# Kernel optimization log

Measured on AMD Instinct MI355X. Metric: run time of the kernel, lower is better.

## Reference

```python
import jax, jax.numpy as jnp
import numpy as np

EPS = 1e-8


def setup_inputs() -> dict:
    key = jax.random.key(0)
    k1, k2 = jax.random.split(key)
    N, F, K, C = 100000, 32, 16, 10
    membership = jax.nn.softmax(jax.random.normal(k1, (N, F, K), jnp.float32), axis=2)
    teacher_probs = jax.nn.softmax(jax.random.normal(k2, (N, C), jnp.float32), axis=1)
    return {"membership": membership, "teacher_probs": teacher_probs}


def _soft_losses(membership, teacher_probs):
    N, F, K = membership.shape
    bin_mass = membership.sum(axis=0) + EPS                       # (F,K)
    # centroids[f,k,c] = sum_n membership[n,f,k]*y[n,c] / mass[f,k]
    centroids = jnp.einsum('nfk,nc->fkc', membership, teacher_probs) / bin_mass[..., None]
    # ||y_n - c_fk||^2 = ||y||^2 + ||c||^2 - 2 y.c  (avoids O(NFKC) broadcast)
    y_sq = jnp.sum(teacher_probs * teacher_probs, axis=1)          # (N,)
    c_sq = jnp.sum(centroids * centroids, axis=2)                  # (F,K)
    cross = jnp.einsum('nc,fkc->nfk', teacher_probs, centroids)    # (N,F,K)
    sq_dist = y_sq[:, None, None] + c_sq[None, :, :] - 2.0 * cross
    loss_intra = jnp.sum(membership * sq_dist) / N
    inter = jnp.sum((centroids[:, :-1, :] - centroids[:, 1:, :]) ** 2)
    loss_inter = -1.0 * inter / F
    return loss_intra, loss_inter


def _hard_variance(membership, teacher_probs):
    N, F, K = membership.shape
    hard = jnp.argmax(membership, axis=2)                          # (N,F)
    onehot = (hard[:, :, None] == jnp.arange(K)[None, None, :]).astype(teacher_probs.dtype)  # (N,F,K)
    counts = onehot.sum(axis=0)                                    # (F,K)
    sum_y = jnp.einsum('nfk,nc->fkc', onehot, teacher_probs)       # (F,K,C)
    y_sq = jnp.sum(teacher_probs * teacher_probs, axis=1)          # (N,)
    sumsq = jnp.einsum('nfk,n->fk', onehot, y_sq)                  # (F,K)
    safe = jnp.maximum(counts, 1.0)
    centroid = sum_y / safe[..., None]                             # (F,K,C)
    c_sq = jnp.sum(centroid * centroid, axis=2)                    # (F,K)
    # mean_n ||y - c||^2 = mean||y||^2 - ||c||^2, only for bins with >1 sample
    bin_var = jnp.where(counts > 1, sumsq / safe - c_sq, 0.0)
    valid_bins = jnp.sum((counts > 1).astype(jnp.float32))
    intra_var = jnp.sum(bin_var) / (valid_bins + EPS)
    # inter: variance of centroids of non-empty bins, per feature
    mask1 = (counts >= 1).astype(teacher_probs.dtype)              # (F,K)
    M = mask1.sum(axis=1)                                          # (F,)
    safe_M = jnp.maximum(M, 1.0)
    mean_c = jnp.sum(centroid * mask1[..., None], axis=1) / safe_M[:, None]  # (F,C)
    dev = (centroid - mean_c[:, None, :]) * mask1[..., None]
    cvar = jnp.sum(dev * dev, axis=(1, 2)) / safe_M                # (F,)
    cvar = jnp.where(M > 1, cvar, 0.0)
    inter_var = jnp.sum(cvar) / F
    return intra_var, inter_var


def reference(membership, teacher_probs):
    loss_intra, loss_inter = _soft_losses(membership, teacher_probs)
    intra_var, inter_var = _hard_variance(membership, teacher_probs)
    total = 1.0 * loss_intra + 3.0 * loss_inter
    return (total, loss_intra, loss_inter, intra_var, inter_var)
```

## Files before the change

### kernel.cpp

```cpp
#include <hip/hip_runtime.h>

#define EPSF 1e-8f

constexpr int F  = 32;
constexpr int K  = 16;
constexpr int C  = 10;
constexpr int FK = F * K;
constexpr int OFF_S    = 0;
constexpr int OFF_SY   = FK * C;
constexpr int OFF_MASS = 2 * FK * C;
constexpr int OFF_CNT  = OFF_MASS + FK;
constexpr int OFF_SSQ  = OFF_CNT + FK;
constexpr int OFF_YQM  = OFF_SSQ + FK;
constexpr int REP      = OFF_YQM + 1;
constexpr int RG       = 16;

typedef float f32x10 __attribute__((ext_vector_type(10)));

#define K1_STEP(NN, MM) do {                                              \
    const int ns_ = __builtin_amdgcn_readfirstlane(NN);                   \
    const float* yr_ = yp + (size_t)ns_ * C;                              \
    f32x10 yv_;                                                           \
    _Pragma("unroll")                                                     \
    for (int c = 0; c < C; ++c) yv_[c] = yr_[c];                          \
    float ysq_ = 0.f;                                                     \
    _Pragma("unroll")                                                     \
    for (int c = 0; c < C; ++c) ysq_ += yv_[c] * yv_[c];                  \
    _Pragma("unroll")                                                     \
    for (int c = 0; c < C; ++c) { S0[c] += (MM).x * yv_[c];               \
                                  S1[c] += (MM).y * yv_[c]; }             \
    mass0 += (MM).x; mass1 += (MM).y;                                     \
    yqm   += ((MM).x + (MM).y) * ysq_;                                    \
    float bm_; int bk_;                                                   \
    if ((MM).y > (MM).x) { bm_ = (MM).y; bk_ = k2 + 1; }                  \
    else                 { bm_ = (MM).x; bk_ = k2;     }                  \
    _Pragma("unroll")                                                     \
    for (int off = 1; off < 8; off <<= 1) {                               \
        const float om_ = __shfl_xor(bm_, off);                           \
        const int   ok_ = __shfl_xor(bk_, off);                           \
        if (om_ > bm_ || (om_ == bm_ && ok_ < bk_)) { bm_ = om_; bk_ = ok_; } \
    }                                                                     \
    if (bk_ == k2) {                                                      \
        cnt0 += 1.f; ssq0 += ysq_;                                        \
        _Pragma("unroll")                                                 \
        for (int c = 0; c < C; ++c) Y0[c] += yv_[c];                      \
    } else if (bk_ == k2 + 1) {                                           \
        cnt1 += 1.f; ssq1 += ysq_;                                        \
        _Pragma("unroll")                                                 \
        for (int c = 0; c < C; ++c) Y1[c] += yv_[c];                      \
    }                                                                     \
} while (0)

__global__ __launch_bounds__(512, 2) void k1_accum(const float* __restrict__ mem,
                                                   const float* __restrict__ yp,
                                                   float* __restrict__ ws,
                                                   int N, int chunk)
{
    const int t    = threadIdx.x;
    const int slot = t & 255;
    const int h    = t >> 8;
    const int b    = blockIdx.x;
    const int k2   = (slot & 7) * 2;

    f32x10 S0, S1, Y0, Y1;
#pragma unroll
    for (int c = 0; c < C; ++c) { S0[c] = 0.f; S1[c] = 0.f; Y0[c] = 0.f; Y1[c] = 0.f; }
    float mass0 = 0.f, mass1 = 0.f, cnt0 = 0.f, cnt1 = 0.f, ssq0 = 0.f, ssq1 = 0.f;
    float yqm = 0.f;

    const int start = b * chunk;
    const int end   = min(N, start + chunk);
    const float* mslot = mem + (size_t)slot * 2;

    int n0 = start;
    for (; n0 + 7 < end; n0 += 8) {
        const float2 m0 = *reinterpret_cast<const float2*>(mslot + (size_t)(n0 + h)     * FK);
        const float2 m1 = *reinterpret_cast<const float2*>(mslot + (size_t)(n0 + 2 + h) * FK);
        const float2 m2 = *reinterpret_cast<const float2*>(mslot + (size_t)(n0 + 4 + h) * FK);
        const float2 m3 = *reinterpret_cast<const float2*>(mslot + (size_t)(n0 + 6 + h) * FK);
        K1_STEP(n0 + h,     m0);
        K1_STEP(n0 + 2 + h, m1);
        K1_STEP(n0 + 4 + h, m2);
        K1_STEP(n0 + 6 + h, m3);
    }
    for (; n0 < end; n0 += 2) {
        const int n = n0 + h;
        if (n < end) {
            const float2 mt = *reinterpret_cast<const float2*>(mslot + (size_t)n * FK);
            K1_STEP(n, mt);
        }
    }

    __shared__ float wsum[8];
    float yq = yqm;
#pragma unroll
    for (int off = 1; off < 64; off <<= 1) yq += __shfl_xor(yq, off);
    if ((t & 63) == 0) wsum[t >> 6] = yq;

    __shared__ float lds[256 * 46];
    if (h == 1) {
        float* q = &lds[slot * 46];
#pragma unroll
        for (int c = 0; c < C; ++c) {
            q[c]      = S0[c];  q[10 + c] = S1[c];
            q[20 + c] = Y0[c];  q[30 + c] = Y1[c];
        }
        q[40] = mass0; q[41] = mass1;
        q[42] = cnt0;  q[43] = cnt1;
        q[44] = ssq0;  q[45] = ssq1;
    }
    __syncthreads();

    float* rep = ws + (size_t)b * REP;
    if (t == 0) {
        float s = 0.f;
        for (int w = 0; w < 8; ++w) s += wsum[w];
        rep[OFF_YQM] = s;
    }
    if (h == 0) {
        const float* q = &lds[slot * 46];
        const int fk0 = slot * 2, fk1 = slot * 2 + 1;
#pragma unroll
        for (int c = 0; c < C; ++c) {
            rep[OFF_S  + fk0 * C + c] = S0[c] + q[c];
            rep[OFF_S  + fk1 * C + c] = S1[c] + q[10 + c];
            rep[OFF_SY + fk0 * C + c] = Y0[c] + q[20 + c];
            rep[OFF_SY + fk1 * C + c] = Y1[c] + q[30 + c];
        }
        rep[OFF_MASS + fk0] = mass0 + q[40]; rep[OFF_MASS + fk1] = mass1 + q[41];
        rep[OFF_CNT  + fk0] = cnt0  + q[42]; rep[OFF_CNT  + fk1] = cnt1  + q[43];
        rep[OFF_SSQ  + fk0] = ssq0  + q[44]; rep[OFF_SSQ  + fk1] = ssq1  + q[45];
    }
}

__global__ __launch_bounds__(256) void k2_reduce(const float* __restrict__ ws,
                                                 float* __restrict__ partial,
                                                 int G, int CH)
{
    const int e = blockIdx.x * 256 + threadIdx.x;
    if (e >= REP) return;
    const int g  = blockIdx.y;
    const int r0 = g * CH;
    const int r1 = min(G, r0 + CH);
    float s0 = 0.f, s1 = 0.f, s2 = 0.f, s3 = 0.f;
    int r = r0;
    for (; r + 3 < r1; r += 4) {
        s0 += ws[(size_t)(r + 0) * REP + e];
        s1 += ws[(size_t)(r + 1) * REP + e];
        s2 += ws[(size_t)(r + 2) * REP + e];
        s3 += ws[(size_t)(r + 3) * REP + e];
    }
    for (; r < r1; ++r) s0 += ws[(size_t)r * REP + e];
    partial[(size_t)g * REP + e] = (s0 + s1) + (s2 + s3);
}

__global__ __launch_bounds__(256) void k2b_collapse(const float* __restrict__ partial,
                                                    float* __restrict__ red)
{
    const int e = blockIdx.x * 256 + threadIdx.x;
    if (e >= REP) return;
    float s = 0.f;
#pragma unroll
    for (int g = 0; g < RG; ++g) s += partial[(size_t)g * REP + e];
    red[e] = s;
}

__global__ __launch_bounds__(512) void k3_final(const float* __restrict__ red,
                                                float* __restrict__ out, float Nf)
{
    const int t = threadIdx.x;
    const int k = t & (K - 1);

    const float* Sa = red + OFF_S;
    const float* Ya = red + OFF_SY;
    const float* Ma = red + OFF_MASS;
    const float* Ca = red + OFF_CNT;
    const float* Qa = red + OFF_SSQ;
    const float  yqm = red[OFF_YQM];

    const float massr = Ma[t];
    const float bmass = massr + EPSF;
    float cen[C], csq = 0.f, Cp = 0.f;
#pragma unroll
    for (int c = 0; c < C; ++c) {
        const float s  = Sa[t * C + c];
        const float cc = s / bmass;
        cen[c] = cc; csq += cc * cc; Cp += cc * s;
    }
    const float q1 = csq * massr - 2.f * Cp;

    __shared__ float sC[FK][C];
#pragma unroll
    for (int c = 0; c < C; ++c) sC[t][c] = cen[c];
    __syncthreads();
    float interp = 0.f;
    if (k < K - 1) {
#pragma unroll
        for (int c = 0; c < C; ++c) { const float d = cen[c] - sC[t + 1][c]; interp += d * d; }
    }

    const float cntv = Ca[t];
    const float safe = fmaxf(cntv, 1.f);
    float cenh[C], csqh = 0.f;
#pragma unroll
    for (int c = 0; c < C; ++c) { const float v = Ya[t * C + c] / safe; cenh[c] = v; csqh += v * v; }
    const float binv  = (cntv > 1.f) ? (Qa[t] / safe - csqh) : 0.f;
    const float valid = (cntv > 1.f) ? 1.f : 0.f;
    const float m1    = (cntv >= 1.f) ? 1.f : 0.f;

    float M = m1;
#pragma unroll
    for (int off = 1; off < 16; off <<= 1) M += __shfl_xor(M, off);
    const float safeM = fmaxf(M, 1.f);
    float dev2 = 0.f;
#pragma unroll
    for (int c = 0; c < C; ++c) {
        float v = cenh[c] * m1;
#pragma unroll
        for (int off = 1; off < 16; off <<= 1) v += __shfl_xor(v, off);
        const float d = (cenh[c] - v / safeM) * m1;
        dev2 += d * d;
    }
#pragma unroll
    for (int off = 1; off < 16; off <<= 1) dev2 += __shfl_xor(dev2, off);
    const float cvar  = (M > 1.f) ? dev2 / safeM : 0.f;
    const float cvar0 = (k == 0) ? cvar : 0.f;

    float vals[5] = { q1, interp, binv, valid, cvar0 };
    __shared__ float rbuf[8][5];
#pragma unroll
    for (int i = 0; i < 5; ++i) {
        float v = vals[i];
#pragma unroll
        for (int off = 1; off < 64; off <<= 1) v += __shfl_xor(v, off);
        if ((t & 63) == 0) rbuf[t >> 6][i] = v;
    }
    __syncthreads();
    if (t == 0) {
        float s[5] = {0.f, 0.f, 0.f, 0.f, 0.f};
        for (int w = 0; w < 8; ++w)
            for (int i = 0; i < 5; ++i) s[i] += rbuf[w][i];
        const float loss_intra = (yqm + s[0]) / Nf;
        const float loss_inter = -s[1] / (float)F;
        const float intra_var  = s[2] / (s[3] + EPSF);
        const float inter_var  = s[4] / (float)F;
        out[0] = loss_intra + 3.f * loss_inter;
        out[1] = loss_intra;
        out[2] = loss_inter;
        out[3] = intra_var;
        out[4] = inter_var;
    }
}

extern "C" void kernel_launch(void* const* d_in, const int* in_sizes, int n_in,
                              void* d_out, int out_size, void* d_ws, size_t ws_size,
                              hipStream_t stream)
{
    (void)n_in; (void)out_size;
    const float* mem = (const float*)d_in[0];
    const float* yp  = (const float*)d_in[1];
    float* out = (float*)d_out;
    const int N = in_sizes[0] / FK;

    int G = 512;
    {
        const size_t need = ((size_t)G + RG + 1) * REP * sizeof(float);
        if (need > ws_size) {
            G = (int)(ws_size / sizeof(float) / REP) - (RG + 1);
            if (G < 1) G = 1;
            if (G > 512) G = 512;
        }
    }
    float* ws      = (float*)d_ws;
    float* partial = ws + (size_t)G * REP;
    float* red     = partial + (size_t)RG * REP;
    const int chunk = (N + G - 1) / G;
    const int CH    = (G + RG - 1) / RG;

    k1_accum<<<G, 512, 0, stream>>>(mem, yp, ws, N, chunk);
    k2_reduce<<<dim3((REP + 255) / 256, RG), 256, 0, stream>>>(ws, partial, G, CH);
    k2b_collapse<<<(REP + 255) / 256, 256, 0, stream>>>(partial, red);
    k3_final<<<1, 512, 0, stream>>>(red, out, (float)N);
}
```

Baseline: 328.8 us.

## Restructure accumulation kernel to 256-thread blocks with DPP argmax and more grid blocks

The accumulation kernel now uses 256 threads per block, each owning two (f,k) bins for every row, and drops the two-half split along with its LDS merge of partial sums. The grid doubles to 1024 blocks and the reduce stage uses 32 groups. The 8-lane argmax shuffles become DPP moves (quad permutes plus row_shr/shl selected by lane), and teacher rows are read as float2 vectors. The aim is less cross-lane and LDS overhead and more blocks in flight, at the cost of a larger workspace for the reduce stage to read.

```diff
diff --git a/kernel.cpp b/kernel.cpp
--- a/kernel.cpp
+++ b/kernel.cpp
@@ -13,54 +13,60 @@
 constexpr int OFF_SSQ  = OFF_CNT + FK;
 constexpr int OFF_YQM  = OFF_SSQ + FK;
 constexpr int REP      = OFF_YQM + 1;
-constexpr int RG       = 16;
+constexpr int RG       = 32;
+constexpr int G1       = 1024;
 
 typedef float f32x10 __attribute__((ext_vector_type(10)));
 
-#define K1_STEP(NN, MM) do {                                              \
-    const int ns_ = __builtin_amdgcn_readfirstlane(NN);                   \
-    const float* yr_ = yp + (size_t)ns_ * C;                              \
-    f32x10 yv_;                                                           \
-    _Pragma("unroll")                                                     \
-    for (int c = 0; c < C; ++c) yv_[c] = yr_[c];                          \
-    float ysq_ = 0.f;                                                     \
-    _Pragma("unroll")                                                     \
-    for (int c = 0; c < C; ++c) ysq_ += yv_[c] * yv_[c];                  \
-    _Pragma("unroll")                                                     \
-    for (int c = 0; c < C; ++c) { S0[c] += (MM).x * yv_[c];               \
-                                  S1[c] += (MM).y * yv_[c]; }             \
-    mass0 += (MM).x; mass1 += (MM).y;                                     \
-    yqm   += ((MM).x + (MM).y) * ysq_;                                    \
-    float bm_; int bk_;                                                   \
-    if ((MM).y > (MM).x) { bm_ = (MM).y; bk_ = k2 + 1; }                  \
-    else                 { bm_ = (MM).x; bk_ = k2;     }                  \
-    _Pragma("unroll")                                                     \
-    for (int off = 1; off < 8; off <<= 1) {                               \
-        const float om_ = __shfl_xor(bm_, off);                           \
-        const int   ok_ = __shfl_xor(bk_, off);                           \
-        if (om_ > bm_ || (om_ == bm_ && ok_ < bk_)) { bm_ = om_; bk_ = ok_; } \
-    }                                                                     \
-    if (bk_ == k2) {                                                      \
-        cnt0 += 1.f; ssq0 += ysq_;                                        \
-        _Pragma("unroll")                                                 \
-        for (int c = 0; c < C; ++c) Y0[c] += yv_[c];                      \
-    } else if (bk_ == k2 + 1) {                                           \
-        cnt1 += 1.f; ssq1 += ysq_;                                        \
-        _Pragma("unroll")                                                 \
-        for (int c = 0; c < C; ++c) Y1[c] += yv_[c];                      \
-    }                                                                     \
+#define DPPF(x, ctrl) __int_as_float(__builtin_amdgcn_mov_dpp(__float_as_int(x), (ctrl), 0xF, 0xF, true))
+#define DPPI(x, ctrl) __builtin_amdgcn_mov_dpp((x), (ctrl), 0xF, 0xF, true)
+
+#define LOADY(NN, YV) do {                                                   \
+    const float2* yr_ = reinterpret_cast<const float2*>(yp + (size_t)(NN) * C); \
+    const float2 a_ = yr_[0], b_ = yr_[1], c2_ = yr_[2], d_ = yr_[3], e_ = yr_[4]; \
+    (YV)[0] = a_.x; (YV)[1] = a_.y; (YV)[2] = b_.x; (YV)[3] = b_.y;          \
+    (YV)[4] = c2_.x; (YV)[5] = c2_.y; (YV)[6] = d_.x; (YV)[7] = d_.y;        \
+    (YV)[8] = e_.x; (YV)[9] = e_.y;                                          \
 } while (0)
 
-__global__ __launch_bounds__(512, 2) void k1_accum(const float* __restrict__ mem,
-                                                   const float* __restrict__ yp,
-                                                   float* __restrict__ ws,
-                                                   int N, int chunk)
-{
-    const int t    = threadIdx.x;
-    const int slot = t & 255;
-    const int h    = t >> 8;
-    const int b    = blockIdx.x;
-    const int k2   = (slot & 7) * 2;
+#define K1_STEP(MM, YV, YSQ) do {                                            \
+    _Pragma("unroll")                                                        \
+    for (int c = 0; c < C; ++c) { S0[c] += (MM).x * (YV)[c];                 \
+                                  S1[c] += (MM).y * (YV)[c]; }               \
+    mass0 += (MM).x; mass1 += (MM).y;                                        \
+    yqm   += ((MM).x + (MM).y) * (YSQ);                                      \
+    float bm_; int bk_;                                                      \
+    if ((MM).y > (MM).x) { bm_ = (MM).y; bk_ = k2 + 1; }                     \
+    else                 { bm_ = (MM).x; bk_ = k2;     }                     \
+    { const float om_ = DPPF(bm_, 0xB1); const int ok_ = DPPI(bk_, 0xB1);    \
+      if (om_ > bm_ || (om_ == bm_ && ok_ < bk_)) { bm_ = om_; bk_ = ok_; } } \
+    { const float om_ = DPPF(bm_, 0x4E); const int ok_ = DPPI(bk_, 0x4E);    \
+      if (om_ > bm_ || (om_ == bm_ && ok_ < bk_)) { bm_ = om_; bk_ = ok_; } } \
+    { const float oa_ = DPPF(bm_, 0x124); const float ob_ = DPPF(bm_, 0x12C); \
+      const int   ka_ = DPPI(bk_, 0x124); const int   kb_ = DPPI(bk_, 0x12C); \
+      const float om_ = hi4 ? ob_ : oa_;  const int   ok_ = hi4 ? kb_ : ka_; \
+      if (om_ > bm_ || (om_ == bm_ && ok_ < bk_)) { bm_ = om_; bk_ = ok_; } } \
+    if (bk_ == k2) {                                                         \
+        cnt0 += 1.f; ssq0 += (YSQ);                                          \
+        _Pragma("unroll")                                                    \
+        for (int c = 0; c < C; ++c) Y0[c] += (YV)[c];                        \
+    } else if (bk_ == k2 + 1) {                                              \
+        cnt1 += 1.f; ssq1 += (YSQ);                                          \
+        _Pragma("unroll")                                                    \
+        for (int c = 0; c < C; ++c) Y1[c] += (YV)[c];                        \
+    }                                                                        \
+} while (0)
+
+__global__ __launch_bounds__(256) void k1_accum(const float* __restrict__ mem,
+                                                const float* __restrict__ yp,
+                                                float* __restrict__ ws,
+                                                int N, int chunk)
+{
+    const int t     = threadIdx.x;
+    const int b     = blockIdx.x;
+    const int k2    = (t & 7) * 2;
+    const int slot2 = t * 2;
+    const bool hi4  = (t & 4) != 0;
 
     f32x10 S0, S1, Y0, Y1;
 #pragma unroll
@@ -70,67 +76,51 @@
 
     const int start = b * chunk;
     const int end   = min(N, start + chunk);
-    const float* mslot = mem + (size_t)slot * 2;
-
-    int n0 = start;
-    for (; n0 + 7 < end; n0 += 8) {
-        const float2 m0 = *reinterpret_cast<const float2*>(mslot + (size_t)(n0 + h)     * FK);
-        const float2 m1 = *reinterpret_cast<const float2*>(mslot + (size_t)(n0 + 2 + h) * FK);
-        const float2 m2 = *reinterpret_cast<const float2*>(mslot + (size_t)(n0 + 4 + h) * FK);
-        const float2 m3 = *reinterpret_cast<const float2*>(mslot + (size_t)(n0 + 6 + h) * FK);
-        K1_STEP(n0 + h,     m0);
-        K1_STEP(n0 + 2 + h, m1);
-        K1_STEP(n0 + 4 + h, m2);
-        K1_STEP(n0 + 6 + h, m3);
-    }
-    for (; n0 < end; n0 += 2) {
-        const int n = n0 + h;
-        if (n < end) {
-            const float2 mt = *reinterpret_cast<const float2*>(mslot + (size_t)n * FK);
-            K1_STEP(n, mt);
-        }
-    }
-
-    __shared__ float wsum[8];
+
+    int n = start;
+    for (; n + 1 < end; n += 2) {
+        const float2 ma = *reinterpret_cast<const float2*>(mem + (size_t)n       * FK + slot2);
+        const float2 mb = *reinterpret_cast<const float2*>(mem + (size_t)(n + 1) * FK + slot2);
+        f32x10 yva, yvb;
+        LOADY(n, yva);
+        LOADY(n + 1, yvb);
+        float ysqa = 0.f, ysqb = 0.f;
+#pragma unroll
+        for (int c = 0; c < C; ++c) { ysqa += yva[c] * yva[c]; ysqb += yvb[c] * yvb[c]; }
+        K1_STEP(ma, yva, ysqa);
+        K1_STEP(mb, yvb, ysqb);
+    }
+    if (n < end) {
+        const float2 ma = *reinterpret_cast<const float2*>(mem + (size_t)n * FK + slot2);
+        f32x10 yva;
+        LOADY(n, yva);
+        float ysqa = 0.f;
+#pragma unroll
+        for (int c = 0; c < C; ++c) ysqa += yva[c] * yva[c];
+        K1_STEP(ma, yva, ysqa);
+    }
+
+    __shared__ float wsum[4];
     float yq = yqm;
 #pragma unroll
     for (int off = 1; off < 64; off <<= 1) yq += __shfl_xor(yq, off);
     if ((t & 63) == 0) wsum[t >> 6] = yq;
-
-    __shared__ float lds[256 * 46];
-    if (h == 1) {
-        float* q = &lds[slot * 46];
-#pragma unroll
-        for (int c = 0; c < C; ++c) {
-            q[c]      = S0[c];  q[10 + c] = S1[c];
-            q[20 + c] = Y0[c];  q[30 + c] = Y1[c];
-        }
-        q[40] = mass0; q[41] = mass1;
-        q[42] = cnt0;  q[43] = cnt1;
-        q[44] = ssq0;  q[45] = ssq1;
-    }
     __syncthreads();
 
     float* rep = ws + (size_t)b * REP;
-    if (t == 0) {
-        float s = 0.f;
-        for (int w = 0; w < 8; ++w) s += wsum[w];
-        rep[OFF_YQM] = s;
-    }
-    if (h == 0) {
-        const float* q = &lds[slot * 46];
-        const int fk0 = slot * 2, fk1 = slot * 2 + 1;
-#pragma unroll
-        for (int c = 0; c < C; ++c) {
-            rep[OFF_S  + fk0 * C + c] = S0[c] + q[c];
-            rep[OFF_S  + fk1 * C + c] = S1[c] + q[10 + c];
-            rep[OFF_SY + fk0 * C + c] = Y0[c] + q[20 + c];
-            rep[OFF_SY + fk1 * C + c] = Y1[c] + q[30 + c];
-        }
-        rep[OFF_MASS + fk0] = mass0 + q[40]; rep[OFF_MASS + fk1] = mass1 + q[41];
-        rep[OFF_CNT  + fk0] = cnt0  + q[42]; rep[OFF_CNT  + fk1] = cnt1  + q[43];
-        rep[OFF_SSQ  + fk0] = ssq0  + q[44]; rep[OFF_SSQ  + fk1] = ssq1  + q[45];
-    }
+    if (t == 0) rep[OFF_YQM] = (wsum[0] + wsum[1]) + (wsum[2] + wsum[3]);
+
+    const int fk0 = slot2, fk1 = slot2 + 1;
+#pragma unroll
+    for (int c = 0; c < C; ++c) {
+        rep[OFF_S  + fk0 * C + c] = S0[c];
+        rep[OFF_S  + fk1 * C + c] = S1[c];
+        rep[OFF_SY + fk0 * C + c] = Y0[c];
+        rep[OFF_SY + fk1 * C + c] = Y1[c];
+    }
+    rep[OFF_MASS + fk0] = mass0; rep[OFF_MASS + fk1] = mass1;
+    rep[OFF_CNT  + fk0] = cnt0;  rep[OFF_CNT  + fk1] = cnt1;
+    rep[OFF_SSQ  + fk0] = ssq0;  rep[OFF_SSQ  + fk1] = ssq1;
 }
 
 __global__ __launch_bounds__(256) void k2_reduce(const float* __restrict__ ws,
@@ -262,13 +252,13 @@
     float* out = (float*)d_out;
     const int N = in_sizes[0] / FK;
 
-    int G = 512;
+    int G = G1;
     {
         const size_t need = ((size_t)G + RG + 1) * REP * sizeof(float);
         if (need > ws_size) {
             G = (int)(ws_size / sizeof(float) / REP) - (RG + 1);
             if (G < 1) G = 1;
-            if (G > 512) G = 512;
+            if (G > G1) G = G1;
         }
     }
     float* ws      = (float*)d_ws;
@@ -277,7 +267,7 @@
     const int chunk = (N + G - 1) / G;
     const int CH    = (G + RG - 1) / RG;
 
-    k1_accum<<<G, 512, 0, stream>>>(mem, yp, ws, N, chunk);
+    k1_accum<<<G, 256, 0, stream>>>(mem, yp, ws, N, chunk);
     k2_reduce<<<dim3((REP + 255) / 256, RG), 256, 0, stream>>>(ws, partial, G, CH);
     k2b_collapse<<<(REP + 255) / 256, 256, 0, stream>>>(partial, red);
     k3_final<<<1, 512, 0, stream>>>(red, out, (float)N);
```

Result: no change. 327.9 us (-0.3%).
